# Kernel optimization log

Hardware: AMD Instinct MI355X
Metric: run time of the kernel (lower is better)

## Reference

```python
import jax, jax.numpy as jnp
import numpy as np

NUM_HEADS = 8


def setup_inputs() -> dict:
    key = jax.random.key(0)
    k1, k2, k3 = jax.random.split(key, 3)
    B, C, D, H, W = 2, 512, 32, 32, 32
    x = jax.random.normal(k1, (B, C, D, H, W), dtype=jnp.float32)
    w_qkv = jax.random.normal(k2, (3 * C, C), dtype=jnp.float32) * 0.02
    b_qkv = jnp.zeros((3 * C,), dtype=jnp.float32)
    w_out = jax.random.normal(k3, (C, C), dtype=jnp.float32) * 0.02
    b_out = jnp.zeros((C,), dtype=jnp.float32)
    return {"x": x, "w_qkv": w_qkv, "b_qkv": b_qkv, "w_out": w_out, "b_out": b_out}


def reference(x, w_qkv, b_qkv, w_out, b_out):
    B, C, D, H, W = x.shape
    nh = NUM_HEADS
    hd = C // nh
    # 1x1x1 conv3d == pointwise linear over channel dim
    qkv = jnp.einsum('bcdhw,oc->bodhw', x, w_qkv) + b_qkv[None, :, None, None, None]
    q, k, v = jnp.split(qkv, 3, axis=1)  # each [B,C,D,H,W]

    def to_heads(t):
        # [B,C,D,H,W] -> [B,nh,hd,D,H,W] -> [B,H,W,nh,D,hd]
        return t.reshape(B, nh, hd, D, H, W).transpose(0, 4, 5, 1, 3, 2)

    q, k, v = to_heads(q), to_heads(k), to_heads(v)
    scale = hd ** -0.5
    # attention along the depth axis D: attn [B,H,W,nh,D,D]
    attn = jnp.einsum('bhwnic,bhwnjc->bhwnij', q, k) * scale
    attn = jax.nn.softmax(attn, axis=-1)
    out = jnp.einsum('bhwnij,bhwnjc->bhwnic', attn, v)  # [B,H,W,nh,D,hd]
    # [B,H,W,nh,D,hd] -> [B,nh,hd,D,H,W] -> [B,C,D,H,W]
    out = out.transpose(0, 3, 5, 4, 1, 2).reshape(B, C, D, H, W)
    out = jnp.einsum('bcdhw,oc->bodhw', out, w_out) + b_out[None, :, None, None, None]
    return out + x
```

## Files before the change

### kernel.cpp

```cpp
#include <hip/hip_runtime.h>


typedef __bf16 bf16x8 __attribute__((ext_vector_type(8)));
typedef float  f32x4  __attribute__((ext_vector_type(4)));
typedef float  f32x16 __attribute__((ext_vector_type(16)));

__device__ __forceinline__ float b2f(unsigned int u) {
    union { float f; unsigned int i; } x; x.i = u << 16; return x.f;
}
__device__ __forceinline__ unsigned short f2b(float f) {
    union { float f; unsigned int i; } x; x.f = f;
    unsigned int r = x.i + 0x7FFFu + ((x.i >> 16) & 1u);
    return (unsigned short)(r >> 16);
}
__device__ __forceinline__ unsigned int cvtpk(float lo, float hi) {
    unsigned int r;
    asm("v_cvt_pk_bf16_f32 %0, %1, %2" : "=v"(r) : "v"(lo), "v"(hi));
    return r;
}
__device__ __forceinline__ f32x4 mfma16(bf16x8 a, bf16x8 b, f32x4 c) {
    return __builtin_amdgcn_mfma_f32_16x16x32_bf16(a, b, c, 0, 0, 0);
}
__device__ __forceinline__ f32x16 mfma32(bf16x8 a, bf16x8 b, f32x16 c) {
    return __builtin_amdgcn_mfma_f32_32x32x16_bf16(a, b, c, 0, 0, 0);
}
__device__ __forceinline__ void gload16(const void* g, void* l) {
    __builtin_amdgcn_global_load_lds((const unsigned int*)g, (unsigned int*)l, 16, 0, 0);
}

__global__ __launch_bounds__(256) void xprep(const float* __restrict__ x,
                                             const float* __restrict__ wq_f,
                                             const float* __restrict__ wo_f,
                                             unsigned short* __restrict__ xT,
                                             unsigned short* __restrict__ wbf) {
    const int bid = blockIdx.x;
    const int t   = threadIdx.x;
    if (bid >= 2048) {
        int i0 = (bid - 2048) * 1024 + t;
        #pragma unroll
        for (int k = 0; k < 4; ++k) {
            int i = i0 + k * 256;
            const float* src;
            int off;
            if (i < 196608) { src = wq_f; off = i * 4; }
            else            { src = wo_f; off = (i - 196608) * 4; }
            float4 v = *(const float4*)(src + off);
            *(uint2*)(wbf + (size_t)i * 4) = make_uint2(cvtpk(v.x, v.y), cvtpk(v.z, v.w));
        }
        return;
    }
    __shared__ __align__(16) char tile[32768];
    const int c0 = (bid & 7) * 64;
    const int s0 = (bid >> 3) * 256;
    const int b  = s0 >> 15;
    const int sp = s0 & 32767;

    const float* px = x + (size_t)b * 16777216 + (size_t)(c0 + (t & 7) * 8) * 32768 + sp + (t >> 3) * 8;
    float va[8][8];
    #pragma unroll
    for (int j = 0; j < 8; ++j) {
        float4 a0 = *(const float4*)(px + (size_t)j * 32768);
        float4 a1 = *(const float4*)(px + (size_t)j * 32768 + 4);
        va[j][0] = a0.x; va[j][1] = a0.y; va[j][2] = a0.z; va[j][3] = a0.w;
        va[j][4] = a1.x; va[j][5] = a1.y; va[j][6] = a1.z; va[j][7] = a1.w;
    }
    #pragma unroll
    for (int k = 0; k < 8; ++k) {
        uint4 o = make_uint4(cvtpk(va[0][k], va[1][k]), cvtpk(va[2][k], va[3][k]),
                             cvtpk(va[4][k], va[5][k]), cvtpk(va[6][k], va[7][k]));
        const int srow = (t >> 3) * 8 + k;
        *(uint4*)(tile + srow * 128 + (((t & 7) ^ k) << 4)) = o;
    }
    __syncthreads();
    unsigned short* dst = xT + (size_t)(s0 + t) * 512 + c0;
    #pragma unroll
    for (int m = 0; m < 8; ++m) {
        uint4 v = *(const uint4*)(tile + t * 128 + ((m ^ (t & 7)) << 4));
        *(uint4*)(dst + m * 8) = v;
    }
}

__global__ __launch_bounds__(256, 2)
void axial_ab(const unsigned short* __restrict__ xT,
              const unsigned short* __restrict__ wq,
              const float* __restrict__ bq,
              unsigned short* __restrict__ ao)
{
    __shared__ __align__(16) char lds[81920];
    const int QT0 = 0, KT0 = 16384, VT0 = 32768, P0 = 49152, BIAS0 = 57344;
    float* bias_s = (float*)(lds + BIAS0);

    const int bid = blockIdx.x;
    const int vid = (bid & 7) * 512 + (bid >> 3);
    const int n   = vid & 7;
    const int tg  = vid >> 3;
    const int b   = tg >> 8;
    const int h   = (tg >> 3) & 31;
    const int w0  = (tg & 7) * 4;
    const int sbase = b * 32768 + h * 32 + w0;

    const int tid = threadIdx.x;
    const int wv  = tid >> 6;
    const int l   = tid & 63;
    const int l31 = l & 31;
    const int hh  = l >> 5;
    const int wm  = wv >> 1;
    const int wn  = wv & 1;

    auto stage = [&](int kk, int buf) {
        #pragma unroll
        for (int i = 0; i < 6; ++i) {
            const int il  = wv * 6 + i;
            const int row = il * 8 + (l >> 3);
            const int R   = n * 64 + (row & 63) + ((row >> 6) << 9);
            const unsigned short* src = wq + R * 512 + kk * 64 + (((l & 7) ^ (row & 7)) << 3);
            gload16(src, lds + buf * 24576 + il * 1024);
        }
        #pragma unroll
        for (int i = 0; i < 4; ++i) {
            const int il  = wv * 4 + i;
            const int row = il * 8 + (l >> 3);
            const int d   = row & 31;
            const int wr  = row >> 5;
            const int s   = sbase + d * 1024 + wr;
            const unsigned short* src = xT + (size_t)s * 512 + kk * 64 + (((l & 7) ^ (row & 7)) << 3);
            gload16(src, lds + 49152 + buf * 16384 + il * 1024);
        }
    };

    f32x16 acc[3][2];
    #pragma unroll
    for (int mf = 0; mf < 3; ++mf)
        #pragma unroll
        for (int nf = 0; nf < 2; ++nf) acc[mf][nf] = (f32x16)0.f;

    stage(0, 0);
    __syncthreads();
    int cur = 0;
    for (int kk = 0; kk < 8; ++kk) {
        if (kk < 7) stage(kk + 1, cur ^ 1);
        #pragma unroll
        for (int ks = 0; ks < 4; ++ks) {
            bf16x8 af[3], bfr[2];
            #pragma unroll
            for (int mf = 0; mf < 3; ++mf) {
                const int row = wm * 96 + mf * 32 + l31;
                af[mf] = *(const bf16x8*)(lds + cur * 24576 + row * 128 +
                                          (((ks * 2 + hh) ^ (row & 7)) << 4));
            }
            #pragma unroll
            for (int nf = 0; nf < 2; ++nf) {
                const int row = wn * 64 + nf * 32 + l31;
                bfr[nf] = *(const bf16x8*)(lds + 49152 + cur * 16384 + row * 128 +
                                           (((ks * 2 + hh) ^ (row & 7)) << 4));
            }
            #pragma unroll
            for (int mf = 0; mf < 3; ++mf)
                #pragma unroll
                for (int nf = 0; nf < 2; ++nf)
                    acc[mf][nf] = mfma32(af[mf], bfr[nf], acc[mf][nf]);
        }
        __syncthreads();
        cur ^= 1;
    }

    if (tid < 192) bias_s[tid] = bq[((tid >> 6) << 9) + n * 64 + (tid & 63)];
    __syncthreads();

    #pragma unroll
    for (int mf = 0; mf < 3; ++mf) {
        const int m0 = wm * 96 + mf * 32;
        #pragma unroll
        for (int nf = 0; nf < 2; ++nf) {
            const int t = wn * 2 + nf;
            const f32x16 v = acc[mf][nf];
            if (m0 < 128) {
                const int base = (m0 < 64) ? QT0 : KT0;
                const int c0g  = (m0 & 63) >> 3;
                const int d    = l31;
                #pragma unroll
                for (int p = 0; p < 4; ++p) {
                    float4 bb = *(const float4*)(bias_s + m0 + 8 * p + 4 * hh);
                    unsigned int u0 = cvtpk(v[4 * p]     + bb.x, v[4 * p + 1] + bb.y);
                    unsigned int u1 = cvtpk(v[4 * p + 2] + bb.z, v[4 * p + 3] + bb.w);
                    *(uint2*)(lds + base + t * 4096 + d * 128 +
                              (((c0g + p) ^ (d & 7)) << 4) + 8 * hh) = make_uint2(u0, u1);
                }
            } else {
                const int e0 = m0 - 128;
                const int j  = wn * 64 + nf * 32 + l31;
                #pragma unroll
                for (int reg = 0; reg < 16; ++reg) {
                    const int e = e0 + (reg & 3) + 8 * (reg >> 2) + 4 * hh;
                    unsigned int u = cvtpk(v[reg], v[reg]);
                    *(unsigned short*)(lds + VT0 + e * 256 +
                                       (((j >> 3) ^ (e & 7)) << 4) + ((2 * j) & 15)) =
                        (unsigned short)(u & 0xffffu);
                }
            }
        }
    }
    __syncthreads();

    {
        const int t  = wv;
        const int qg = l >> 4;
        f32x4 sacc[2][2];
        sacc[0][0] = (f32x4)0.f; sacc[0][1] = (f32x4)0.f;
        sacc[1][0] = (f32x4)0.f; sacc[1][1] = (f32x4)0.f;
        #pragma unroll
        for (int kh = 0; kh < 2; ++kh) {
            bf16x8 qa[2], kb[2];
            #pragma unroll
            for (int mt = 0; mt < 2; ++mt) {
                const int i = mt * 16 + (l & 15);
                qa[mt] = *(const bf16x8*)(lds + QT0 + t * 4096 + i * 128 +
                                          (((kh * 4 + qg) ^ (i & 7)) << 4));
            }
            #pragma unroll
            for (int nt = 0; nt < 2; ++nt) {
                const int jj = nt * 16 + (l & 15);
                kb[nt] = *(const bf16x8*)(lds + KT0 + t * 4096 + jj * 128 +
                                          (((kh * 4 + qg) ^ (jj & 7)) << 4));
            }
            #pragma unroll
            for (int mt = 0; mt < 2; ++mt)
                #pragma unroll
                for (int nt = 0; nt < 2; ++nt)
                    sacc[mt][nt] = mfma16(qa[mt], kb[nt], sacc[mt][nt]);
        }
        #pragma unroll
        for (int mt = 0; mt < 2; ++mt) {
            #pragma unroll
            for (int reg = 0; reg < 4; ++reg) {
                float s0 = sacc[mt][0][reg] * 0.125f;
                float s1 = sacc[mt][1][reg] * 0.125f;
                float m = fmaxf(s0, s1);
                m = fmaxf(m, __shfl_xor(m, 1));
                m = fmaxf(m, __shfl_xor(m, 2));
                m = fmaxf(m, __shfl_xor(m, 4));
                m = fmaxf(m, __shfl_xor(m, 8));
                float p0 = __expf(s0 - m);
                float p1 = __expf(s1 - m);
                float ss = p0 + p1;
                ss += __shfl_xor(ss, 1);
                ss += __shfl_xor(ss, 2);
                ss += __shfl_xor(ss, 4);
                ss += __shfl_xor(ss, 8);
                float inv = 1.0f / ss;
                const int i = mt * 16 + 4 * qg + reg;
                #pragma unroll
                for (int nt = 0; nt < 2; ++nt) {
                    const int j = nt * 16 + (l & 15);
                    unsigned int u = cvtpk((nt ? p1 : p0) * inv, 0.f);
                    *(unsigned short*)(lds + P0 + t * 2048 + i * 64 +
                                       (((j >> 3) ^ (i & 3)) << 4) + ((2 * j) & 15)) =
                        (unsigned short)(u & 0xffffu);
                }
            }
        }
        asm volatile("s_waitcnt lgkmcnt(0)" ::: "memory");
        __builtin_amdgcn_sched_barrier(0);

        f32x16 oa[2];
        oa[0] = (f32x16)0.f; oa[1] = (f32x16)0.f;
        #pragma unroll
        for (int ks = 0; ks < 2; ++ks) {
            bf16x8 pb = *(const bf16x8*)(lds + P0 + t * 2048 + l31 * 64 +
                                         (((ks * 2 + hh) ^ (l31 & 3)) << 4));
            #pragma unroll
            for (int cf = 0; cf < 2; ++cf) {
                const int c = cf * 32 + l31;
                bf16x8 vv = *(const bf16x8*)(lds + VT0 + c * 256 +
                                             (((t * 4 + ks * 2 + hh) ^ (c & 7)) << 4));
                oa[cf] = mfma32(vv, pb, oa[cf]);
            }
        }
        const size_t srow = (size_t)(sbase + l31 * 1024 + t) * 512 + n * 64;
        #pragma unroll
        for (int cf = 0; cf < 2; ++cf) {
            #pragma unroll
            for (int p = 0; p < 4; ++p) {
                const int cb = cf * 32 + 8 * p + 4 * hh;
                float4 bb = *(const float4*)(bias_s + 128 + cb);
                unsigned int u0 = cvtpk(oa[cf][4 * p]     + bb.x, oa[cf][4 * p + 1] + bb.y);
                unsigned int u1 = cvtpk(oa[cf][4 * p + 2] + bb.z, oa[cf][4 * p + 3] + bb.w);
                *(uint2*)(ao + srow + cb) = make_uint2(u0, u1);
            }
        }
    }
}

__global__ __launch_bounds__(256, 2)
void axial_out(const unsigned short* __restrict__ ao,
               const unsigned short* __restrict__ wo,
               const float* __restrict__ bo,
               const float* __restrict__ x,
               float* __restrict__ out)
{
    __shared__ __align__(16) char lds[65536];
    const int bid = blockIdx.x;
    const int vid = (bid & 7) * 256 + (bid >> 3);
    const int mt_ = vid & 3;
    const int nt_ = vid >> 2;
    const int m_base = mt_ * 128;
    const int s_base = nt_ * 128;
    const int bb  = s_base >> 15;
    const int spl = s_base & 32767;
    const float* xblk = x + (size_t)bb * 16777216 + spl;
    float* oblk = out + (size_t)bb * 16777216 + spl;

    const int tid = threadIdx.x;
    const int wv  = tid >> 6;
    const int l   = tid & 63;
    const int l31 = l & 31;
    const int hh  = l >> 5;
    const int wm  = wv >> 1;
    const int wn  = wv & 1;

    auto stage = [&](int kk, int buf) {
        #pragma unroll
        for (int i = 0; i < 4; ++i) {
            const int il  = wv * 4 + i;
            const int row = il * 8 + (l >> 3);
            const unsigned short* srcA = wo + (m_base + row) * 512 + kk * 64 +
                                         (((l & 7) ^ (row & 7)) << 3);
            gload16(srcA, lds + buf * 16384 + il * 1024);
            const unsigned short* srcB = ao + (size_t)(s_base + row) * 512 + kk * 64 +
                                         (((l & 7) ^ (row & 7)) << 3);
            gload16(srcB, lds + 32768 + buf * 16384 + il * 1024);
        }
    };

    f32x16 acc[2][2];
    acc[0][0] = (f32x16)0.f; acc[0][1] = (f32x16)0.f;
    acc[1][0] = (f32x16)0.f; acc[1][1] = (f32x16)0.f;

    stage(0, 0);
    __syncthreads();
    int cur = 0;
    for (int kk = 0; kk < 8; ++kk) {
        if (kk < 7) stage(kk + 1, cur ^ 1);
        #pragma unroll
        for (int ks = 0; ks < 4; ++ks) {
            bf16x8 af[2], bfr[2];
            #pragma unroll
            for (int mf = 0; mf < 2; ++mf) {
                const int row = wm * 64 + mf * 32 + l31;
                af[mf] = *(const bf16x8*)(lds + cur * 16384 + row * 128 +
                                          (((ks * 2 + hh) ^ (row & 7)) << 4));
            }
            #pragma unroll
            for (int nf = 0; nf < 2; ++nf) {
                const int row = wn * 64 + nf * 32 + l31;
                bfr[nf] = *(const bf16x8*)(lds + 32768 + cur * 16384 + row * 128 +
                                           (((ks * 2 + hh) ^ (row & 7)) << 4));
            }
            #pragma unroll
            for (int mf = 0; mf < 2; ++mf)
                #pragma unroll
                for (int nf = 0; nf < 2; ++nf)
                    acc[mf][nf] = mfma32(af[mf], bfr[nf], acc[mf][nf]);
        }
        __syncthreads();
        cur ^= 1;
    }

    #pragma unroll
    for (int mf = 0; mf < 2; ++mf) {
        #pragma unroll
        for (int reg = 0; reg < 16; ++reg) {
            const int co = m_base + wm * 64 + mf * 32 + (reg & 3) + 8 * (reg >> 2) + 4 * hh;
            const float bias = bo[co];
            #pragma unroll
            for (int nf = 0; nf < 2; ++nf) {
                const int sl = wn * 64 + nf * 32 + l31;
                oblk[(size_t)co * 32768 + sl] = acc[mf][nf][reg] + bias +
                                                xblk[(size_t)co * 32768 + sl];
            }
        }
    }
}

__device__ __forceinline__ int adr_qk(int row, int cb) { return row * 2048 + (cb ^ ((row & 7) << 4)); }
__device__ __forceinline__ int adr_x (int row, int cb) { return 98304 + row * 1024 + (cb ^ ((row & 7) << 4)); }
__device__ __forceinline__ int adr_xl(int row, int cb) { return 131072 + row * 1024 + (cb ^ ((row & 7) << 4)); }
__device__ __forceinline__ int adr_v (int e, int jb)   { int a = e * 64 + jb; return 65536 + (a ^ ((e & 7) << 4)); }

__global__ __launch_bounds__(512, 1)
void axial3d_mfma(const float* __restrict__ x,
                  const float* __restrict__ bq,
                  const float* __restrict__ bo,
                  const unsigned short* __restrict__ wq,
                  const unsigned short* __restrict__ wo,
                  float* __restrict__ out) {
    __shared__ char lds[163840];
    const int bid  = blockIdx.x;
    const int work = (bid & 7) * 256 + (bid >> 3);
    const int b    = work >> 10;
    const int h    = (work >> 5) & 31;
    const int w    = work & 31;
    const float* xb = x   + ((size_t)b * 16777216u) + h * 32 + w;
    float*       ob = out + ((size_t)b * 16777216u) + h * 32 + w;
    const int tid  = threadIdx.x;
    const int wv   = tid >> 6;
    const int lane = tid & 63;
    const int g    = lane >> 4;
    const int q    = lane & 15;
    {
        const int d  = tid & 31;
        const int c0 = tid >> 5;
        #pragma unroll
        for (int it = 0; it < 32; ++it) {
            int c = c0 + it * 16;
            float xv = xb[c * 32768 + d * 1024];
            unsigned short hi = f2b(xv);
            unsigned short lo = f2b(xv - b2f(hi));
            *(unsigned short*)(lds + adr_x(d, c * 2))  = hi;
            *(unsigned short*)(lds + adr_xl(d, c * 2)) = lo;
        }
    }
    __syncthreads();
    for (int tp = 0; tp < 3; ++tp) {
        const int mt0 = wv * 12 + tp * 4;
        f32x4 acc[4][2];
        #pragma unroll
        for (int t = 0; t < 4; ++t) { acc[t][0] = (f32x4)0.f; acc[t][1] = (f32x4)0.f; }
        #pragma unroll
        for (int kk = 0; kk < 16; ++kk) {
            bf16x8 bfr[2];
            #pragma unroll
            for (int nt = 0; nt < 2; ++nt)
                bfr[nt] = *(const bf16x8*)(lds + adr_x(nt * 16 + q, kk * 64 + g * 16));
            #pragma unroll
            for (int t = 0; t < 4; ++t) {
                const int o = (mt0 + t) * 16 + q;
                bf16x8 a = *(const bf16x8*)((const char*)wq + o * 1024 + kk * 64 + g * 16);
                acc[t][0] = mfma16(a, bfr[0], acc[t][0]);
                acc[t][1] = mfma16(a, bfr[1], acc[t][1]);
            }
        }
        #pragma unroll
        for (int t = 0; t < 4; ++t) {
            const int mt    = mt0 + t;
            const int obase = mt * 16 + 4 * g;
            float bias[4];
            #pragma unroll
            for (int r = 0; r < 4; ++r) bias[r] = bq[obase + r];
            if (mt < 64) {
                #pragma unroll
                for (int nt = 0; nt < 2; ++nt) {
                    const int d = nt * 16 + q;
                    unsigned int lo = f2b(acc[t][nt][0] + bias[0]) |
                                      ((unsigned int)f2b(acc[t][nt][1] + bias[1]) << 16);
                    unsigned int hi = f2b(acc[t][nt][2] + bias[2]) |
                                      ((unsigned int)f2b(acc[t][nt][3] + bias[3]) << 16);
                    *(uint2*)(lds + adr_qk(d, obase * 2)) = make_uint2(lo, hi);
                }
            } else {
                #pragma unroll
                for (int nt = 0; nt < 2; ++nt) {
                    const int d = nt * 16 + q;
                    #pragma unroll
                    for (int r = 0; r < 4; ++r) {
                        const int e = obase + r - 1024;
                        *(unsigned short*)(lds + adr_v(e, d * 2)) = f2b(acc[t][nt][r] + bias[r]);
                    }
                }
            }
        }
    }
    __syncthreads();
    {
        const int n = wv;
        f32x4 s[2][2];
        s[0][0] = (f32x4)0.f; s[0][1] = (f32x4)0.f;
        s[1][0] = (f32x4)0.f; s[1][1] = (f32x4)0.f;
        #pragma unroll
        for (int kk = 0; kk < 2; ++kk) {
            bf16x8 a0 = *(const bf16x8*)(lds + adr_qk(q,      n * 128 + kk * 64 + g * 16));
            bf16x8 a1 = *(const bf16x8*)(lds + adr_qk(16 + q, n * 128 + kk * 64 + g * 16));
            bf16x8 b0 = *(const bf16x8*)(lds + adr_qk(q,      1024 + n * 128 + kk * 64 + g * 16));
            bf16x8 b1 = *(const bf16x8*)(lds + adr_qk(16 + q, 1024 + n * 128 + kk * 64 + g * 16));
            s[0][0] = mfma16(a0, b0, s[0][0]);
            s[0][1] = mfma16(a0, b1, s[0][1]);
            s[1][0] = mfma16(a1, b0, s[1][0]);
            s[1][1] = mfma16(a1, b1, s[1][1]);
        }
        float pv[2][2][4];
        #pragma unroll
        for (int it = 0; it < 2; ++it) {
            #pragma unroll
            for (int r = 0; r < 4; ++r) {
                float s0 = s[it][0][r] * 0.125f;
                float s1 = s[it][1][r] * 0.125f;
                float m = fmaxf(s0, s1);
                m = fmaxf(m, __shfl_xor(m, 1));
                m = fmaxf(m, __shfl_xor(m, 2));
                m = fmaxf(m, __shfl_xor(m, 4));
                m = fmaxf(m, __shfl_xor(m, 8));
                float p0 = __expf(s0 - m);
                float p1 = __expf(s1 - m);
                float ss = p0 + p1;
                ss += __shfl_xor(ss, 1);
                ss += __shfl_xor(ss, 2);
                ss += __shfl_xor(ss, 4);
                ss += __shfl_xor(ss, 8);
                float inv = 1.0f / ss;
                pv[it][0][r] = p0 * inv;
                pv[it][1][r] = p1 * inv;
            }
        }
        #pragma unroll
        for (int it = 0; it < 2; ++it)
            #pragma unroll
            for (int jt = 0; jt < 2; ++jt)
                #pragma unroll
                for (int r = 0; r < 4; ++r) {
                    const int i = it * 16 + 4 * g + r;
                    *(unsigned short*)(lds + adr_qk(i, n * 128 + (jt * 16 + q) * 2)) =
                        f2b(pv[it][jt][r]);
                }
        asm volatile("s_waitcnt lgkmcnt(0)" ::: "memory");
        __builtin_amdgcn_sched_barrier(0);
        bf16x8 pa0 = *(const bf16x8*)(lds + adr_qk(q,      n * 128 + g * 16));
        bf16x8 pa1 = *(const bf16x8*)(lds + adr_qk(16 + q, n * 128 + g * 16));
        #pragma unroll
        for (int et = 0; et < 4; ++et) {
            const int e = n * 64 + et * 16 + q;
            bf16x8 vb = *(const bf16x8*)(lds + adr_v(e, g * 16));
            f32x4 o0 = mfma16(pa0, vb, (f32x4)0.f);
            f32x4 o1 = mfma16(pa1, vb, (f32x4)0.f);
            const int cb = 1024 + n * 128 + (et * 16 + q) * 2;
            #pragma unroll
            for (int r = 0; r < 4; ++r) {
                *(unsigned short*)(lds + adr_qk(4 * g + r, cb))      = f2b(o0[r]);
                *(unsigned short*)(lds + adr_qk(16 + 4 * g + r, cb)) = f2b(o1[r]);
            }
        }
    }
    __syncthreads();
    for (int p4 = 0; p4 < 4; ++p4) {
        const int mt = wv * 4 + p4;
        f32x4 acc[2];
        acc[0] = (f32x4)0.f; acc[1] = (f32x4)0.f;
        #pragma unroll
        for (int kk = 0; kk < 16; ++kk) {
            bf16x8 b0 = *(const bf16x8*)(lds + adr_qk(q,      1024 + kk * 64 + g * 16));
            bf16x8 b1 = *(const bf16x8*)(lds + adr_qk(16 + q, 1024 + kk * 64 + g * 16));
            bf16x8 a  = *(const bf16x8*)((const char*)wo + (mt * 16 + q) * 1024 + kk * 64 + g * 16);
            acc[0] = mfma16(a, b0, acc[0]);
            acc[1] = mfma16(a, b1, acc[1]);
        }
        const int obase = mt * 16 + 4 * g;
        float bias[4];
        #pragma unroll
        for (int r = 0; r < 4; ++r) bias[r] = bo[obase + r];
        #pragma unroll
        for (int nt = 0; nt < 2; ++nt) {
            const int d = nt * 16 + q;
            uint2 xh = *(const uint2*)(lds + adr_x(d, obase * 2));
            uint2 xl = *(const uint2*)(lds + adr_xl(d, obase * 2));
            float res[4];
            res[0] = b2f(xh.x & 0xffffu) + b2f(xl.x & 0xffffu);
            res[1] = b2f(xh.x >> 16)     + b2f(xl.x >> 16);
            res[2] = b2f(xh.y & 0xffffu) + b2f(xl.y & 0xffffu);
            res[3] = b2f(xh.y >> 16)     + b2f(xl.y >> 16);
            #pragma unroll
            for (int r = 0; r < 4; ++r)
                ob[(obase + r) * 32768 + d * 1024] = acc[nt][r] + bias[r] + res[r];
        }
    }
}

extern "C" void kernel_launch(void* const* d_in, const int* in_sizes, int n_in,
                              void* d_out, int out_size, void* d_ws, size_t ws_size,
                              hipStream_t stream) {
    const float* x     = (const float*)d_in[0];
    const float* w_qkv = (const float*)d_in[1];
    const float* b_qkv = (const float*)d_in[2];
    const float* w_out = (const float*)d_in[3];
    const float* b_out = (const float*)d_in[4];
    float* out = (float*)d_out;

    const size_t XT_OFF = 0;
    const size_t AO_OFF = 67108864;
    const size_t WQ_OFF = 134217728;
    const size_t NEED   = 136314880;

    if (ws_size >= NEED) {
        unsigned short* xT  = (unsigned short*)((char*)d_ws + XT_OFF);
        unsigned short* ao  = (unsigned short*)((char*)d_ws + AO_OFF);
        unsigned short* wbf = (unsigned short*)((char*)d_ws + WQ_OFF);
        xprep   <<<dim3(2304), dim3(256), 0, stream>>>(x, w_qkv, w_out, xT, wbf);
        axial_ab<<<dim3(4096), dim3(256), 0, stream>>>(xT, wbf, b_qkv, ao);
        axial_out<<<dim3(2048), dim3(256), 0, stream>>>(ao, wbf + 786432, b_out, x, out);
    } else {
        unsigned short* wbf = (unsigned short*)d_ws;
        xprep<<<dim3(2304), dim3(256), 0, stream>>>(x, (const float*)d_in[1], w_out,
                                                    (unsigned short*)d_ws, wbf);
        axial3d_mfma<<<dim3(2048), dim3(512), 0, stream>>>(x, b_qkv, b_out,
                                                           wbf, wbf + 786432, out);
    }
}
```

Measured before the change: 278.4 us.

## Deepen QKV GEMM pipeline to four-stage ring with smaller K tiles

The QKV projection's K loop now uses K-tiles of 32 instead of 64 and a 4-slot LDS ring with three tiles in flight, replacing the double buffer. Explicit vmcnt waits and raw s_barrier take the place of __syncthreads, so the loop waits only for the oldest tile. The swizzle is adapted to the 64-byte rows, and s_setprio raises priority around the MFMA phase. The goal is to hide global-load latency behind MFMA work. The cost is twice as many barriers and more fragile hand-counted waitcnt logic.

```diff
diff --git a/kernel.cpp b/kernel.cpp
--- a/kernel.cpp
+++ b/kernel.cpp
@@ -107,24 +107,26 @@
     const int wm  = wv >> 1;
     const int wn  = wv & 1;
 
-    auto stage = [&](int kk, int buf) {
-        #pragma unroll
-        for (int i = 0; i < 6; ++i) {
-            const int il  = wv * 6 + i;
-            const int row = il * 8 + (l >> 3);
-            const int R   = n * 64 + (row & 63) + ((row >> 6) << 9);
-            const unsigned short* src = wq + R * 512 + kk * 64 + (((l & 7) ^ (row & 7)) << 3);
-            gload16(src, lds + buf * 24576 + il * 1024);
-        }
-        #pragma unroll
-        for (int i = 0; i < 4; ++i) {
-            const int il  = wv * 4 + i;
-            const int row = il * 8 + (l >> 3);
-            const int d   = row & 31;
-            const int wr  = row >> 5;
-            const int s   = sbase + d * 1024 + wr;
-            const unsigned short* src = xT + (size_t)s * 512 + kk * 64 + (((l & 7) ^ (row & 7)) << 3);
-            gload16(src, lds + 49152 + buf * 16384 + il * 1024);
+    auto stage = [&](int k, int slot) {
+        #pragma unroll
+        for (int i = 0; i < 3; ++i) {
+            const int il = wv * 3 + i;
+            const int r  = il * 16 + (l >> 2);
+            const int R  = n * 64 + (r & 63) + ((r >> 6) << 9);
+            const unsigned short* src = wq + R * 512 + k * 32 +
+                                        (((l & 3) ^ ((r >> 1) & 3)) << 3);
+            gload16(src, lds + slot * 12288 + il * 1024);
+        }
+        #pragma unroll
+        for (int i = 0; i < 2; ++i) {
+            const int il = wv * 2 + i;
+            const int r  = il * 16 + (l >> 2);
+            const int d  = r & 31;
+            const int wr = r >> 5;
+            const int s  = sbase + d * 1024 + wr;
+            const unsigned short* src = xT + (size_t)s * 512 + k * 32 +
+                                        (((l & 3) ^ ((r >> 1) & 3)) << 3);
+            gload16(src, lds + 49152 + slot * 8192 + il * 1024);
         }
     };
 
@@ -134,25 +136,21 @@
         #pragma unroll
         for (int nf = 0; nf < 2; ++nf) acc[mf][nf] = (f32x16)0.f;
 
-    stage(0, 0);
-    __syncthreads();
-    int cur = 0;
-    for (int kk = 0; kk < 8; ++kk) {
-        if (kk < 7) stage(kk + 1, cur ^ 1);
-        #pragma unroll
-        for (int ks = 0; ks < 4; ++ks) {
+    auto gphase = [&](int slot) {
+        #pragma unroll
+        for (int ks = 0; ks < 2; ++ks) {
             bf16x8 af[3], bfr[2];
             #pragma unroll
             for (int mf = 0; mf < 3; ++mf) {
-                const int row = wm * 96 + mf * 32 + l31;
-                af[mf] = *(const bf16x8*)(lds + cur * 24576 + row * 128 +
-                                          (((ks * 2 + hh) ^ (row & 7)) << 4));
+                const int r = wm * 96 + mf * 32 + l31;
+                af[mf] = *(const bf16x8*)(lds + slot * 12288 + r * 64 +
+                                          (((ks * 2 + hh) ^ ((r >> 1) & 3)) << 4));
             }
             #pragma unroll
             for (int nf = 0; nf < 2; ++nf) {
-                const int row = wn * 64 + nf * 32 + l31;
-                bfr[nf] = *(const bf16x8*)(lds + 49152 + cur * 16384 + row * 128 +
-                                           (((ks * 2 + hh) ^ (row & 7)) << 4));
+                const int r = wn * 64 + nf * 32 + l31;
+                bfr[nf] = *(const bf16x8*)(lds + 49152 + slot * 8192 + r * 64 +
+                                           (((ks * 2 + hh) ^ ((r >> 1) & 3)) << 4));
             }
             #pragma unroll
             for (int mf = 0; mf < 3; ++mf)
@@ -160,8 +158,25 @@
                 for (int nf = 0; nf < 2; ++nf)
                     acc[mf][nf] = mfma32(af[mf], bfr[nf], acc[mf][nf]);
         }
-        __syncthreads();
-        cur ^= 1;
+    };
+
+    stage(0, 0); stage(1, 1); stage(2, 2);
+    asm volatile("s_waitcnt vmcnt(10)" ::: "memory");
+    __builtin_amdgcn_s_barrier();
+    __builtin_amdgcn_sched_barrier(0);
+
+    #pragma unroll
+    for (int k = 0; k < 16; ++k) {
+        if (k < 13) stage(k + 3, (k + 3) & 3);
+        __builtin_amdgcn_s_setprio(1);
+        gphase(k & 3);
+        __builtin_amdgcn_s_setprio(0);
+        asm volatile("s_waitcnt lgkmcnt(0)" ::: "memory");
+        if (k < 13)       { asm volatile("s_waitcnt vmcnt(10)" ::: "memory"); }
+        else if (k == 13) { asm volatile("s_waitcnt vmcnt(5)"  ::: "memory"); }
+        else if (k == 14) { asm volatile("s_waitcnt vmcnt(0)"  ::: "memory"); }
+        __builtin_amdgcn_s_barrier();
+        __builtin_amdgcn_sched_barrier(0);
     }
 
     if (tid < 192) bias_s[tid] = bq[((tid >> 6) << 9) + n * 64 + (tid & 63)];
```

After: 282.4 us. About the same (+1.4%).
